# Optimization experiments

Hardware: AMD Instinct MI355X
Metric: run time of the kernel (lower is better)

The kernel has to match this reference:

```python
import jax, jax.numpy as jnp
import numpy as np

K = 128          # fixed max number of points per persistence diagram
BIG = 1e9        # sentinel for masked sort


def _extrema_masks(img):
    # 4-neighborhood local minima / maxima of a 2D image (boundary neighbors = +/-inf)
    p = jnp.pad(img, 1, constant_values=BIG)
    nmin = jnp.minimum(jnp.minimum(p[:-2, 1:-1], p[2:, 1:-1]),
                       jnp.minimum(p[1:-1, :-2], p[1:-1, 2:]))
    q = jnp.pad(img, 1, constant_values=-BIG)
    nmax = jnp.maximum(jnp.maximum(q[:-2, 1:-1], q[2:, 1:-1]),
                       jnp.maximum(q[1:-1, :-2], q[1:-1, 2:]))
    return img <= nmin, img >= nmax


def _diagrams(img):
    # Approximate persistence diagrams of the sublevel-set filtration of img.
    # H0: births at local minima (K smallest), deaths at local maxima (K smallest).
    # H1 (via superlevel duality approx): births at local maxima (K largest),
    #     deaths at local minima (K largest). Fixed cardinality K, invalid slots -> (0,0).
    is_min, is_max = _extrema_masks(img)
    flat = img.ravel()
    mn, mx = is_min.ravel(), is_max.ravel()

    b0 = jnp.sort(jnp.where(mn, flat, BIG))[:K]
    d0 = jnp.sort(jnp.where(mx, flat, BIG))[:K]
    v0 = (b0 < BIG / 2) & (d0 < BIG / 2)
    pd0 = jnp.where(v0[:, None], jnp.stack([b0, jnp.maximum(d0, b0)], -1), 0.0)

    b1 = -jnp.sort(jnp.where(mx, -flat, BIG))[:K]
    d1 = -jnp.sort(jnp.where(mn, -flat, BIG))[:K]
    v1 = (b1 > -BIG / 2) & (d1 > -BIG / 2)
    pd1 = jnp.where(v1[:, None], jnp.stack([b1, jnp.minimum(d1, b1)], -1), 0.0)
    return pd0, pd1


def _w2sq(pa, pb):
    # squared 2-Wasserstein with internal L2, matching points in sorted order
    # (sliced/order-matching approximation of the optimal diagram matching)
    return jnp.sum((pa - pb) ** 2)


def setup_inputs() -> dict:
    key = jax.random.key(0)
    k1, k2 = jax.random.split(key)
    inputs = jax.random.normal(k1, (256, 256, 256), dtype=jnp.float32)
    targets = jax.random.normal(k2, (256, 256, 256), dtype=jnp.float32)
    return {"inputs": inputs, "targets": targets}


def reference(inputs, targets):
    def per_sample(x, y):
        x0, x1 = _diagrams(x)
        y0, y1 = _diagrams(y)
        # wasserstein(pd0)^2 + wasserstein(pd1)^2, as in wasserstein_topological
        return _w2sq(x0, y0) + _w2sq(x1, y1)

    losses = jax.vmap(per_sample)(inputs, targets)  # [B]
    return jnp.mean(losses)  # reduction='mean'
```

## Files before the change

kernel.cpp:

```cpp
#include <hip/hip_runtime.h>
#include <stdint.h>


#define KPTS 128
#define BIGF 1.0e9f
#define IMG_W 256
#define NPIX (IMG_W * IMG_W)
#define NTH 1024
#define QITERS (NPIX / 4 / NTH)
#define LCAP 16384

__device__ __forceinline__ uint32_t f2key(float f) {
    uint32_t u = __float_as_uint(f);
    return (u & 0x80000000u) ? ~u : (u | 0x80000000u);
}
__device__ __forceinline__ float key2f(uint32_t k) {
    uint32_t u = (k & 0x80000000u) ? (k ^ 0x80000000u) : ~k;
    return __uint_as_float(u);
}


struct SMP {
    uint32_t keys[LCAP];
    uint32_t h8[8][256];
    uint32_t cnt[2];
    uint32_t pref[2], rank[2], ccnt[2];
    int      flagAll[2];
    float    buf[4][KPTS];
};

__device__ __forceinline__ void binSelN(const uint32_t (*h)[256], int ncop, int lane, uint32_t r,
                                        uint32_t& bsel, uint32_t& newr) {
    uint32_t b0 = 0, b1 = 0, b2 = 0, b3 = 0;
    for (int c = 0; c < ncop; ++c) {
        b0 += h[c][4 * lane];     b1 += h[c][4 * lane + 1];
        b2 += h[c][4 * lane + 2]; b3 += h[c][4 * lane + 3];
    }
    uint32_t s4 = b0 + b1 + b2 + b3, cum = s4;
    #pragma unroll
    for (int d = 1; d < 64; d <<= 1) { uint32_t t = __shfl_up(cum, d); if (lane >= d) cum += t; }
    unsigned long long m = __ballot(cum > r);
    int L = (m == 0ull) ? 63 : __builtin_ctzll(m);
    uint32_t cumL = __shfl(cum, L), s4L = __shfl(s4, L);
    uint32_t a0 = __shfl(b0, L), a1 = __shfl(b1, L), a2 = __shfl(b2, L);
    uint32_t excl = cumL - s4L;
    if (excl + a0 > r)                { bsel = 4u * L;     newr = r - excl; }
    else if (excl + a0 + a1 > r)      { bsel = 4u * L + 1; newr = r - excl - a0; }
    else if (excl + a0 + a1 + a2 > r) { bsel = 4u * L + 2; newr = r - excl - a0 - a1; }
    else                              { bsel = 4u * L + 3; newr = r - excl - a0 - a1 - a2; }
}

__device__ __forceinline__ void waveSort128(float e[2], bool asc, int lane) {
    for (int size = 2; size <= 128; size <<= 1) {
        for (int stride = size >> 1; stride > 0; stride >>= 1) {
            if (stride == 64) {
                float a = e[0], b = e[1];
                e[0] = asc ? fminf(a, b) : fmaxf(a, b);
                e[1] = asc ? fmaxf(a, b) : fminf(a, b);
            } else {
                #pragma unroll
                for (int r = 0; r < 2; ++r) {
                    int i = r * 64 + lane;
                    float v = e[r];
                    float w = __shfl_xor(v, stride);
                    bool up = ((i & size) == 0) ? asc : !asc;
                    bool lower = (i & stride) == 0;
                    float mn = fminf(v, w), mx = fmaxf(v, w);
                    e[r] = (lower == up) ? mn : mx;
                }
            }
        }
    }
}

__global__ __launch_bounds__(NTH, 8) void topo_pd4_kernel(
        const float* __restrict__ X, const float* __restrict__ Y,
        float* __restrict__ diagOut, uint32_t* __restrict__ gscr, int B) {
    __shared__ SMP sm;
    const int tid = threadIdx.x;
    const int lane = tid & 63;
    const int wv = tid >> 6;
    const int bid = blockIdx.x;
    const float* img = ((bid & 1) ? Y : X) + (size_t)(bid >> 1) * NPIX;
    uint32_t* gmax = gscr + (size_t)bid * LCAP;
    const unsigned long long ltm = (1ull << lane) - 1ull;

    for (int ph = 0; ph < 2; ++ph) {
        for (int i = tid; i < 8 * 256; i += NTH) ((uint32_t*)sm.h8)[i] = 0u;
        if (ph == 0 && tid < 2) sm.cnt[tid] = 0u;
        __syncthreads();
        uint32_t C;

        if (ph == 0) {
            for (int it = 0; it < QITERS; ++it) {
                int q = it * NTH + tid;
                int p = q * 4;
                int row = p >> 8;
                float4 cur = *(const float4*)(img + p);
                bool hu = row > 0, hd = row < (IMG_W - 1);
                float4 up = cur, dn = cur;
                if (hu) up = *(const float4*)(img + p - IMG_W);
                if (hd) dn = *(const float4*)(img + p + IMG_W);
                float lft = __shfl_up(cur.w, 1);
                float rgt = __shfl_down(cur.x, 1);
                bool hl = (lane > 0), hr = (lane < 63);
                float cv[4] = {cur.x, cur.y, cur.z, cur.w};
                float uv[4] = {up.x, up.y, up.z, up.w};
                float dv[4] = {dn.x, dn.y, dn.z, dn.w};
                bool mnf[4], mxf[4];
                uint32_t kk[4];
                #pragma unroll
                for (int j = 0; j < 4; ++j) {
                    float v = cv[j];
                    bool el = (j > 0) || hl, er = (j < 3) || hr;
                    float vl = (j > 0) ? cv[j - 1] : lft;
                    float vr = (j < 3) ? cv[j + 1] : rgt;
                    float nmn = fminf(fminf(el ? vl : BIGF, er ? vr : BIGF),
                                      fminf(hu ? uv[j] : BIGF, hd ? dv[j] : BIGF));
                    float nmx = fmaxf(fmaxf(el ? vl : -BIGF, er ? vr : -BIGF),
                                      fmaxf(hu ? uv[j] : -BIGF, hd ? dv[j] : -BIGF));
                    mnf[j] = (v <= nmn);
                    mxf[j] = (v >= nmx);
                    kk[j] = f2key(v);
                }
                {
                    unsigned long long m0 = __ballot(mnf[0]), m1 = __ballot(mnf[1]),
                                       m2 = __ballot(mnf[2]), m3 = __ballot(mnf[3]);
                    uint32_t c0 = (uint32_t)__popcll(m0), c1 = (uint32_t)__popcll(m1),
                             c2 = (uint32_t)__popcll(m2), c3 = (uint32_t)__popcll(m3);
                    uint32_t base = 0;
                    if (lane == 0) base = atomicAdd(&sm.cnt[0], c0 + c1 + c2 + c3);
                    base = __shfl(base, 0);
                    uint32_t o;
                    if (mnf[0]) { o = base + (uint32_t)__popcll(m0 & ltm);                sm.keys[o < LCAP ? o : LCAP - 1] = kk[0]; atomicAdd(&sm.h8[wv >> 1][kk[0] >> 24], 1u); }
                    if (mnf[1]) { o = base + c0 + (uint32_t)__popcll(m1 & ltm);           sm.keys[o < LCAP ? o : LCAP - 1] = kk[1]; atomicAdd(&sm.h8[wv >> 1][kk[1] >> 24], 1u); }
                    if (mnf[2]) { o = base + c0 + c1 + (uint32_t)__popcll(m2 & ltm);      sm.keys[o < LCAP ? o : LCAP - 1] = kk[2]; atomicAdd(&sm.h8[wv >> 1][kk[2] >> 24], 1u); }
                    if (mnf[3]) { o = base + c0 + c1 + c2 + (uint32_t)__popcll(m3 & ltm); sm.keys[o < LCAP ? o : LCAP - 1] = kk[3]; atomicAdd(&sm.h8[wv >> 1][kk[3] >> 24], 1u); }
                }
                {
                    unsigned long long m0 = __ballot(mxf[0]), m1 = __ballot(mxf[1]),
                                       m2 = __ballot(mxf[2]), m3 = __ballot(mxf[3]);
                    uint32_t c0 = (uint32_t)__popcll(m0), c1 = (uint32_t)__popcll(m1),
                             c2 = (uint32_t)__popcll(m2), c3 = (uint32_t)__popcll(m3);
                    uint32_t base = 0;
                    if (lane == 0) base = atomicAdd(&sm.cnt[1], c0 + c1 + c2 + c3);
                    base = __shfl(base, 0);
                    uint32_t o;
                    if (mxf[0]) { o = base + (uint32_t)__popcll(m0 & ltm);                gmax[o < LCAP ? o : LCAP - 1] = kk[0]; }
                    if (mxf[1]) { o = base + c0 + (uint32_t)__popcll(m1 & ltm);           gmax[o < LCAP ? o : LCAP - 1] = kk[1]; }
                    if (mxf[2]) { o = base + c0 + c1 + (uint32_t)__popcll(m2 & ltm);      gmax[o < LCAP ? o : LCAP - 1] = kk[2]; }
                    if (mxf[3]) { o = base + c0 + c1 + c2 + (uint32_t)__popcll(m3 & ltm); gmax[o < LCAP ? o : LCAP - 1] = kk[3]; }
                }
            }
            __syncthreads();
            C = sm.cnt[0]; if (C > LCAP) C = LCAP;
        } else {
            C = sm.cnt[1]; if (C > LCAP) C = LCAP;
            for (uint32_t i = tid; i < C; i += NTH) {
                uint32_t k = gmax[i];
                sm.keys[i] = k;
                atomicAdd(&sm.h8[wv >> 1][k >> 24], 1u);
            }
            __syncthreads();
        }

        if (wv < 2) {
            bool low = (wv == 0);
            if (C < KPTS) {
                if (lane == 0) { sm.flagAll[wv] = 1; sm.pref[wv] = 0u; sm.rank[wv] = 0u; }
            } else {
                uint32_t bsel, nr;
                binSelN(sm.h8, 8, lane, low ? (KPTS - 1) : (C - KPTS), bsel, nr);
                if (lane == 0) { sm.flagAll[wv] = 0; sm.pref[wv] = bsel; sm.rank[wv] = nr; }
            }
        }
        __syncthreads();

        for (int lvl = 2; lvl >= 0; --lvl) {
            for (int i = tid; i < 2 * 256; i += NTH) ((uint32_t*)sm.h8)[i] = 0u;
            __syncthreads();
            int f0 = sm.flagAll[0], f1 = sm.flagAll[1];
            uint32_t p0 = sm.pref[0], p1 = sm.pref[1];
            const int sp = 8 * (lvl + 1), sb = 8 * lvl;
            for (uint32_t i = tid; i < C; i += NTH) {
                uint32_t k = sm.keys[i], hi = k >> sp, by = (k >> sb) & 255u;
                if (!f0 && hi == p0) atomicAdd(&sm.h8[0][by], 1u);
                if (!f1 && hi == p1) atomicAdd(&sm.h8[1][by], 1u);
            }
            __syncthreads();
            if (wv < 2 && !sm.flagAll[wv]) {
                uint32_t bsel, nr;
                binSelN((const uint32_t(*)[256])&sm.h8[wv], 1, lane, sm.rank[wv], bsel, nr);
                if (lane == 0) { sm.pref[wv] = (sm.pref[wv] << 8) | bsel; sm.rank[wv] = nr; }
            }
            __syncthreads();
        }

        if (tid < 2) sm.ccnt[tid] = 0u;
        __syncthreads();
        const int g0 = (ph == 0) ? 0 : 1;
        const int g1 = (ph == 0) ? 3 : 2;
        {
            int f0 = sm.flagAll[0], f1 = sm.flagAll[1];
            uint32_t t0 = sm.pref[0], t1 = sm.pref[1];
            for (uint32_t i = tid; i < C; i += NTH) {
                uint32_t k = sm.keys[i];
                if (f0 || k < t0) { uint32_t s = atomicAdd(&sm.ccnt[0], 1u); if (s < KPTS) sm.buf[g0][s] = key2f(k); }
                if (f1 || k > t1) { uint32_t s = atomicAdd(&sm.ccnt[1], 1u); if (s < KPTS) sm.buf[g1][s] = key2f(k); }
            }
        }
        __syncthreads();
        if (tid < 2 * KPTS) {
            int l = tid >> 7, i = tid & 127;
            int g = (l == 0) ? g0 : g1;
            if ((uint32_t)i >= sm.ccnt[l])
                sm.buf[g][i] = sm.flagAll[l] ? ((l == 0) ? BIGF : -BIGF) : key2f(sm.pref[l]);
        }
        __syncthreads();
    }

    if (wv < 4) {
        float e[2];
        e[0] = sm.buf[wv][lane];
        e[1] = sm.buf[wv][lane + 64];
        waveSort128(e, wv < 2, lane);
        diagOut[(size_t)bid * 512 + wv * 128 + lane]      = e[0];
        diagOut[(size_t)bid * 512 + wv * 128 + 64 + lane] = e[1];
    }
}

__global__ __launch_bounds__(128) void topo_loss_kernel(
        const float* __restrict__ diag, float* __restrict__ lossOut, int B) {
    const int s = blockIdx.x, i = threadIdx.x;
    const float* xw = diag + (size_t)(2 * s) * 512;
    const float* yw = xw + 512;
    const float H = 0.5f * BIGF;
    float b0x = xw[i], d0x = xw[128 + i], b1x = xw[256 + i], d1x = xw[384 + i];
    float b0y = yw[i], d0y = yw[128 + i], b1y = yw[256 + i], d1y = yw[384 + i];
    bool vx0 = (b0x < H) && (d0x < H);
    float px0b = vx0 ? b0x : 0.f, px0d = vx0 ? fmaxf(d0x, b0x) : 0.f;
    bool vy0 = (b0y < H) && (d0y < H);
    float py0b = vy0 ? b0y : 0.f, py0d = vy0 ? fmaxf(d0y, b0y) : 0.f;
    bool vx1 = (b1x > -H) && (d1x > -H);
    float px1b = vx1 ? b1x : 0.f, px1d = vx1 ? fminf(d1x, b1x) : 0.f;
    bool vy1 = (b1y > -H) && (d1y > -H);
    float py1b = vy1 ? b1y : 0.f, py1d = vy1 ? fminf(d1y, b1y) : 0.f;
    float e0 = px0b - py0b, e1 = px0d - py0d, e2 = px1b - py1b, e3 = px1d - py1d;
    float total = e0 * e0 + e1 * e1 + e2 * e2 + e3 * e3;
    for (int off = 32; off; off >>= 1) total += __shfl_down(total, off);
    __shared__ float lr[2];
    if ((i & 63) == 0) lr[i >> 6] = total;
    __syncthreads();
    if (i == 0) lossOut[s] = lr[0] + lr[1];
}

__global__ void topo_reduce_kernel(const float* __restrict__ ws, float* __restrict__ out, int B) {
    float v = 0.f;
    for (int i = threadIdx.x; i < B; i += 256) v += ws[i];
    __shared__ float r[4];
    for (int off = 32; off; off >>= 1) v += __shfl_down(v, off);
    if ((threadIdx.x & 63) == 0) r[threadIdx.x >> 6] = v;
    __syncthreads();
    if (threadIdx.x == 0) out[0] = (r[0] + r[1] + r[2] + r[3]) / (float)B;
}

__global__ __launch_bounds__(NTH, 8) void topo_pd3_kernel(
        const float* __restrict__ X, const float* __restrict__ Y,
        float* __restrict__ diagOut, int B) {
    __shared__ SMP sm;
    const int tid = threadIdx.x;
    const int lane = tid & 63;
    const int wv = tid >> 6;
    const int bid = blockIdx.x;
    const float* img = ((bid & 1) ? Y : X) + (size_t)(bid >> 1) * NPIX;
    const unsigned long long ltm = (1ull << lane) - 1ull;

    for (int ph = 0; ph < 2; ++ph) {
        for (int i = tid; i < 8 * 256; i += NTH) ((uint32_t*)sm.h8)[i] = 0u;
        if (tid == 0) sm.cnt[0] = 0u;
        __syncthreads();
        for (int it = 0; it < QITERS; ++it) {
            int q = it * NTH + tid;
            int p = q * 4;
            int row = p >> 8;
            float4 cur = *(const float4*)(img + p);
            bool hu = row > 0, hd = row < (IMG_W - 1);
            float4 up = cur, dn = cur;
            if (hu) up = *(const float4*)(img + p - IMG_W);
            if (hd) dn = *(const float4*)(img + p + IMG_W);
            float lft = __shfl_up(cur.w, 1);
            float rgt = __shfl_down(cur.x, 1);
            bool hl = (lane > 0), hr = (lane < 63);
            float cv[4] = {cur.x, cur.y, cur.z, cur.w};
            float uv[4] = {up.x, up.y, up.z, up.w};
            float dv[4] = {dn.x, dn.y, dn.z, dn.w};
            bool e0, e1, e2, e3;
            if (ph == 0) {
                #define SMIN(J, E, EL, ER, VL, VR)                                        \
                    { float nm = fminf(fminf((EL) ? (VL) : BIGF, (ER) ? (VR) : BIGF),     \
                                       fminf(hu ? uv[J] : BIGF, hd ? dv[J] : BIGF));      \
                      E = (cv[J] <= nm); }
                SMIN(0, e0, hl, true, lft,  cv[1]);
                SMIN(1, e1, true, true, cv[0], cv[2]);
                SMIN(2, e2, true, true, cv[1], cv[3]);
                SMIN(3, e3, true, hr, cv[2], rgt);
                #undef SMIN
            } else {
                #define SMAX(J, E, EL, ER, VL, VR)                                        \
                    { float nx = fmaxf(fmaxf((EL) ? (VL) : -BIGF, (ER) ? (VR) : -BIGF),   \
                                       fmaxf(hu ? uv[J] : -BIGF, hd ? dv[J] : -BIGF));    \
                      E = (cv[J] >= nx); }
                SMAX(0, e0, hl, true, lft,  cv[1]);
                SMAX(1, e1, true, true, cv[0], cv[2]);
                SMAX(2, e2, true, true, cv[1], cv[3]);
                SMAX(3, e3, true, hr, cv[2], rgt);
                #undef SMAX
            }
            uint32_t k0 = f2key(cv[0]), k1 = f2key(cv[1]), k2 = f2key(cv[2]), k3 = f2key(cv[3]);
            unsigned long long m0 = __ballot(e0), m1 = __ballot(e1),
                               m2 = __ballot(e2), m3 = __ballot(e3);
            uint32_t c0 = (uint32_t)__popcll(m0), c1 = (uint32_t)__popcll(m1),
                     c2 = (uint32_t)__popcll(m2), c3 = (uint32_t)__popcll(m3);
            uint32_t base = 0;
            if (lane == 0) base = atomicAdd(&sm.cnt[0], c0 + c1 + c2 + c3);
            base = __shfl(base, 0);
            uint32_t o;
            if (e0) { o = base + (uint32_t)__popcll(m0 & ltm);                sm.keys[o < LCAP ? o : LCAP - 1] = k0; atomicAdd(&sm.h8[wv >> 1][k0 >> 24], 1u); }
            if (e1) { o = base + c0 + (uint32_t)__popcll(m1 & ltm);           sm.keys[o < LCAP ? o : LCAP - 1] = k1; atomicAdd(&sm.h8[wv >> 1][k1 >> 24], 1u); }
            if (e2) { o = base + c0 + c1 + (uint32_t)__popcll(m2 & ltm);      sm.keys[o < LCAP ? o : LCAP - 1] = k2; atomicAdd(&sm.h8[wv >> 1][k2 >> 24], 1u); }
            if (e3) { o = base + c0 + c1 + c2 + (uint32_t)__popcll(m3 & ltm); sm.keys[o < LCAP ? o : LCAP - 1] = k3; atomicAdd(&sm.h8[wv >> 1][k3 >> 24], 1u); }
        }
        __syncthreads();
        uint32_t C = sm.cnt[0]; if (C > LCAP) C = LCAP;

        if (wv < 2) {
            bool low = (wv == 0);
            if (C < KPTS) {
                if (lane == 0) { sm.flagAll[wv] = 1; sm.pref[wv] = 0u; sm.rank[wv] = 0u; }
            } else {
                uint32_t bsel, nr;
                binSelN(sm.h8, 8, lane, low ? (KPTS - 1) : (C - KPTS), bsel, nr);
                if (lane == 0) { sm.flagAll[wv] = 0; sm.pref[wv] = bsel; sm.rank[wv] = nr; }
            }
        }
        __syncthreads();

        for (int lvl = 2; lvl >= 0; --lvl) {
            for (int i = tid; i < 2 * 256; i += NTH) ((uint32_t*)sm.h8)[i] = 0u;
            __syncthreads();
            int f0 = sm.flagAll[0], f1 = sm.flagAll[1];
            uint32_t p0 = sm.pref[0], p1 = sm.pref[1];
            const int sp = 8 * (lvl + 1), sb = 8 * lvl;
            for (uint32_t i = tid; i < C; i += NTH) {
                uint32_t k = sm.keys[i], hi = k >> sp, by = (k >> sb) & 255u;
                if (!f0 && hi == p0) atomicAdd(&sm.h8[0][by], 1u);
                if (!f1 && hi == p1) atomicAdd(&sm.h8[1][by], 1u);
            }
            __syncthreads();
            if (wv < 2 && !sm.flagAll[wv]) {
                uint32_t bsel, nr;
                binSelN((const uint32_t(*)[256])&sm.h8[wv], 1, lane, sm.rank[wv], bsel, nr);
                if (lane == 0) { sm.pref[wv] = (sm.pref[wv] << 8) | bsel; sm.rank[wv] = nr; }
            }
            __syncthreads();
        }

        if (tid < 2) sm.ccnt[tid] = 0u;
        __syncthreads();
        const int g0 = (ph == 0) ? 0 : 1;
        const int g1 = (ph == 0) ? 3 : 2;
        {
            int f0 = sm.flagAll[0], f1 = sm.flagAll[1];
            uint32_t t0 = sm.pref[0], t1 = sm.pref[1];
            for (uint32_t i = tid; i < C; i += NTH) {
                uint32_t k = sm.keys[i];
                if (f0 || k < t0) { uint32_t s = atomicAdd(&sm.ccnt[0], 1u); if (s < KPTS) sm.buf[g0][s] = key2f(k); }
                if (f1 || k > t1) { uint32_t s = atomicAdd(&sm.ccnt[1], 1u); if (s < KPTS) sm.buf[g1][s] = key2f(k); }
            }
        }
        __syncthreads();
        if (tid < 2 * KPTS) {
            int l = tid >> 7, i = tid & 127;
            int g = (l == 0) ? g0 : g1;
            if ((uint32_t)i >= sm.ccnt[l])
                sm.buf[g][i] = sm.flagAll[l] ? ((l == 0) ? BIGF : -BIGF) : key2f(sm.pref[l]);
        }
        __syncthreads();
    }

    if (wv < 4) {
        float e[2];
        e[0] = sm.buf[wv][lane];
        e[1] = sm.buf[wv][lane + 64];
        waveSort128(e, wv < 2, lane);
        diagOut[(size_t)bid * 512 + wv * 128 + lane]      = e[0];
        diagOut[(size_t)bid * 512 + wv * 128 + 64 + lane] = e[1];
    }
}

extern "C" void kernel_launch(void* const* d_in, const int* in_sizes, int n_in,
                              void* d_out, int out_size, void* d_ws, size_t ws_size,
                              hipStream_t stream) {
    const float* X = (const float*)d_in[0];
    const float* Y = (const float*)d_in[1];
    float* out = (float*)d_out;
    const int B = in_sizes[0] / NPIX;

    size_t diagSz = (size_t)2 * B * 512 * sizeof(float);
    size_t lossSz = (size_t)B * sizeof(float);
    size_t scrSz  = (size_t)2 * B * LCAP * sizeof(uint32_t);

    if (ws_size >= diagSz + lossSz + scrSz) {
        float* diag = (float*)d_ws;
        float* lossbuf = (float*)((char*)d_ws + diagSz);
        uint32_t* gscr = (uint32_t*)((char*)d_ws + diagSz + lossSz);
        topo_pd4_kernel<<<2 * B, NTH, 0, stream>>>(X, Y, diag, gscr, B);
        topo_loss_kernel<<<B, 128, 0, stream>>>(diag, lossbuf, B);
        topo_reduce_kernel<<<1, 256, 0, stream>>>(lossbuf, out, B);
    } else if (ws_size >= diagSz + lossSz) {
        float* diag = (float*)d_ws;
        float* lossbuf = (float*)((char*)d_ws + diagSz);
        topo_pd3_kernel<<<2 * B, NTH, 0, stream>>>(X, Y, diag, B);
        topo_loss_kernel<<<B, 128, 0, stream>>>(diag, lossbuf, B);
        topo_reduce_kernel<<<1, 256, 0, stream>>>(lossbuf, out, B);
    } else {
        topo_pd3_kernel<<<2 * B, NTH, 0, stream>>>(X, Y, (float*)d_ws, B);
    }
}
```

Baseline: 91.87 us.

## Split extrema scan into grid-wide row kernel and separate selection kernel

The fused per-image kernel, where one 1024-thread block scanned a whole image and then ran radix select, is split in two. A row-parallel scan kernel with 2048 blocks of 256 threads writes the compacted min and max key lists to global memory using global atomic counters. A second kernel per image loads these lists, builds padded, lane-spread shared histograms and performs the selection. This aims to spread the bandwidth-bound scan across the whole GPU and cut shared-atomic contention, at the cost of an extra memset, an extra launch and a global round-trip for the min keys.

Result: slower. 350.6 us (+281.6%).

```diff
diff --git a/kernel.cpp b/kernel.cpp
--- a/kernel.cpp
+++ b/kernel.cpp
@@ -9,6 +9,7 @@
 #define NTH 1024
 #define QITERS (NPIX / 4 / NTH)
 #define LCAP 16384
+#define HPAD 264
 
 __device__ __forceinline__ uint32_t f2key(float f) {
     uint32_t u = __float_as_uint(f);
@@ -20,21 +21,83 @@
 }
 
 
-struct SMP {
+__global__ __launch_bounds__(256) void topo_scan_kernel(
+        const float* __restrict__ X, const float* __restrict__ Y,
+        uint32_t* __restrict__ gkeys, uint32_t* __restrict__ gcnt, int B) {
+    const int tid = threadIdx.x;
+    const int lane = tid & 63;
+    const int wv = tid >> 6;
+    const int gw = blockIdx.x * 4 + wv;
+    const int nw = gridDim.x * 4;
+    const int totalRows = 2 * B * IMG_W;
+    const unsigned long long ltm = (1ull << lane) - 1ull;
+
+    for (int r = gw; r < totalRows; r += nw) {
+        int im = r >> 8, row = r & 255;
+        const float* base = ((im & 1) ? Y : X) + (size_t)(im >> 1) * NPIX + (size_t)row * IMG_W;
+        float4 cur = *(const float4*)(base + lane * 4);
+        bool hu = row > 0, hd = row < (IMG_W - 1);
+        float4 up = cur, dn = cur;
+        if (hu) up = *(const float4*)(base - IMG_W + lane * 4);
+        if (hd) dn = *(const float4*)(base + IMG_W + lane * 4);
+        float lft = __shfl_up(cur.w, 1);
+        float rgt = __shfl_down(cur.x, 1);
+        bool hl = (lane > 0), hr = (lane < 63);
+        float cv[4] = {cur.x, cur.y, cur.z, cur.w};
+        float uv[4] = {up.x, up.y, up.z, up.w};
+        float dv[4] = {dn.x, dn.y, dn.z, dn.w};
+        bool mnf[4], mxf[4];
+        uint32_t kk[4];
+        #pragma unroll
+        for (int j = 0; j < 4; ++j) {
+            float v = cv[j];
+            bool el = (j > 0) || hl, er = (j < 3) || hr;
+            float vl = (j > 0) ? cv[j - 1] : lft;
+            float vr = (j < 3) ? cv[j + 1] : rgt;
+            float nmn = fminf(fminf(el ? vl : BIGF, er ? vr : BIGF),
+                              fminf(hu ? uv[j] : BIGF, hd ? dv[j] : BIGF));
+            float nmx = fmaxf(fmaxf(el ? vl : -BIGF, er ? vr : -BIGF),
+                              fmaxf(hu ? uv[j] : -BIGF, hd ? dv[j] : -BIGF));
+            mnf[j] = (v <= nmn);
+            mxf[j] = (v >= nmx);
+            kk[j] = f2key(v);
+        }
+        #pragma unroll
+        for (int t = 0; t < 2; ++t) {
+            bool f0 = t ? mxf[0] : mnf[0], f1 = t ? mxf[1] : mnf[1];
+            bool f2 = t ? mxf[2] : mnf[2], f3 = t ? mxf[3] : mnf[3];
+            unsigned long long m0 = __ballot(f0), m1 = __ballot(f1),
+                               m2 = __ballot(f2), m3 = __ballot(f3);
+            uint32_t c0 = (uint32_t)__popcll(m0), c1 = (uint32_t)__popcll(m1),
+                     c2 = (uint32_t)__popcll(m2), c3 = (uint32_t)__popcll(m3);
+            uint32_t bse = 0;
+            if (lane == 0) bse = atomicAdd(&gcnt[im * 2 + t], c0 + c1 + c2 + c3);
+            bse = __shfl(bse, 0);
+            uint32_t* dst = gkeys + (size_t)(im * 2 + t) * LCAP;
+            uint32_t o;
+            if (f0) { o = bse + (uint32_t)__popcll(m0 & ltm);                dst[o < LCAP ? o : LCAP - 1] = kk[0]; }
+            if (f1) { o = bse + c0 + (uint32_t)__popcll(m1 & ltm);           dst[o < LCAP ? o : LCAP - 1] = kk[1]; }
+            if (f2) { o = bse + c0 + c1 + (uint32_t)__popcll(m2 & ltm);      dst[o < LCAP ? o : LCAP - 1] = kk[2]; }
+            if (f3) { o = bse + c0 + c1 + c2 + (uint32_t)__popcll(m3 & ltm); dst[o < LCAP ? o : LCAP - 1] = kk[3]; }
+        }
+    }
+}
+
+struct SMQ {
     uint32_t keys[LCAP];
-    uint32_t h8[8][256];
-    uint32_t cnt[2];
+    uint32_t h8[8 * HPAD];
     uint32_t pref[2], rank[2], ccnt[2];
     int      flagAll[2];
     float    buf[4][KPTS];
 };
 
-__device__ __forceinline__ void binSelN(const uint32_t (*h)[256], int ncop, int lane, uint32_t r,
+__device__ __forceinline__ void binSelP(const uint32_t* h, int ncop, int lane, uint32_t r,
                                         uint32_t& bsel, uint32_t& newr) {
     uint32_t b0 = 0, b1 = 0, b2 = 0, b3 = 0;
     for (int c = 0; c < ncop; ++c) {
-        b0 += h[c][4 * lane];     b1 += h[c][4 * lane + 1];
-        b2 += h[c][4 * lane + 2]; b3 += h[c][4 * lane + 3];
+        const uint32_t* hh = h + c * HPAD;
+        b0 += hh[4 * lane];     b1 += hh[4 * lane + 1];
+        b2 += hh[4 * lane + 2]; b3 += hh[4 * lane + 3];
     }
     uint32_t s4 = b0 + b1 + b2 + b3, cum = s4;
     #pragma unroll
@@ -73,96 +136,28 @@
     }
 }
 
-__global__ __launch_bounds__(NTH, 8) void topo_pd4_kernel(
-        const float* __restrict__ X, const float* __restrict__ Y,
-        float* __restrict__ diagOut, uint32_t* __restrict__ gscr, int B) {
-    __shared__ SMP sm;
+__global__ __launch_bounds__(NTH, 8) void topo_sel_kernel(
+        const uint32_t* __restrict__ gkeys, const uint32_t* __restrict__ gcnt,
+        float* __restrict__ diagOut, int B) {
+    __shared__ SMQ sm;
     const int tid = threadIdx.x;
     const int lane = tid & 63;
     const int wv = tid >> 6;
-    const int bid = blockIdx.x;
-    const float* img = ((bid & 1) ? Y : X) + (size_t)(bid >> 1) * NPIX;
-    uint32_t* gmax = gscr + (size_t)bid * LCAP;
-    const unsigned long long ltm = (1ull << lane) - 1ull;
+    const int im = blockIdx.x;
+    const int hc = lane & 7;
 
     for (int ph = 0; ph < 2; ++ph) {
-        for (int i = tid; i < 8 * 256; i += NTH) ((uint32_t*)sm.h8)[i] = 0u;
-        if (ph == 0 && tid < 2) sm.cnt[tid] = 0u;
-        __syncthreads();
-        uint32_t C;
-
-        if (ph == 0) {
-            for (int it = 0; it < QITERS; ++it) {
-                int q = it * NTH + tid;
-                int p = q * 4;
-                int row = p >> 8;
-                float4 cur = *(const float4*)(img + p);
-                bool hu = row > 0, hd = row < (IMG_W - 1);
-                float4 up = cur, dn = cur;
-                if (hu) up = *(const float4*)(img + p - IMG_W);
-                if (hd) dn = *(const float4*)(img + p + IMG_W);
-                float lft = __shfl_up(cur.w, 1);
-                float rgt = __shfl_down(cur.x, 1);
-                bool hl = (lane > 0), hr = (lane < 63);
-                float cv[4] = {cur.x, cur.y, cur.z, cur.w};
-                float uv[4] = {up.x, up.y, up.z, up.w};
-                float dv[4] = {dn.x, dn.y, dn.z, dn.w};
-                bool mnf[4], mxf[4];
-                uint32_t kk[4];
-                #pragma unroll
-                for (int j = 0; j < 4; ++j) {
-                    float v = cv[j];
-                    bool el = (j > 0) || hl, er = (j < 3) || hr;
-                    float vl = (j > 0) ? cv[j - 1] : lft;
-                    float vr = (j < 3) ? cv[j + 1] : rgt;
-                    float nmn = fminf(fminf(el ? vl : BIGF, er ? vr : BIGF),
-                                      fminf(hu ? uv[j] : BIGF, hd ? dv[j] : BIGF));
-                    float nmx = fmaxf(fmaxf(el ? vl : -BIGF, er ? vr : -BIGF),
-                                      fmaxf(hu ? uv[j] : -BIGF, hd ? dv[j] : -BIGF));
-                    mnf[j] = (v <= nmn);
-                    mxf[j] = (v >= nmx);
-                    kk[j] = f2key(v);
-                }
-                {
-                    unsigned long long m0 = __ballot(mnf[0]), m1 = __ballot(mnf[1]),
-                                       m2 = __ballot(mnf[2]), m3 = __ballot(mnf[3]);
-                    uint32_t c0 = (uint32_t)__popcll(m0), c1 = (uint32_t)__popcll(m1),
-                             c2 = (uint32_t)__popcll(m2), c3 = (uint32_t)__popcll(m3);
-                    uint32_t base = 0;
-                    if (lane == 0) base = atomicAdd(&sm.cnt[0], c0 + c1 + c2 + c3);
-                    base = __shfl(base, 0);
-                    uint32_t o;
-                    if (mnf[0]) { o = base + (uint32_t)__popcll(m0 & ltm);                sm.keys[o < LCAP ? o : LCAP - 1] = kk[0]; atomicAdd(&sm.h8[wv >> 1][kk[0] >> 24], 1u); }
-                    if (mnf[1]) { o = base + c0 + (uint32_t)__popcll(m1 & ltm);           sm.keys[o < LCAP ? o : LCAP - 1] = kk[1]; atomicAdd(&sm.h8[wv >> 1][kk[1] >> 24], 1u); }
-                    if (mnf[2]) { o = base + c0 + c1 + (uint32_t)__popcll(m2 & ltm);      sm.keys[o < LCAP ? o : LCAP - 1] = kk[2]; atomicAdd(&sm.h8[wv >> 1][kk[2] >> 24], 1u); }
-                    if (mnf[3]) { o = base + c0 + c1 + c2 + (uint32_t)__popcll(m3 & ltm); sm.keys[o < LCAP ? o : LCAP - 1] = kk[3]; atomicAdd(&sm.h8[wv >> 1][kk[3] >> 24], 1u); }
-                }
-                {
-                    unsigned long long m0 = __ballot(mxf[0]), m1 = __ballot(mxf[1]),
-                                       m2 = __ballot(mxf[2]), m3 = __ballot(mxf[3]);
-                    uint32_t c0 = (uint32_t)__popcll(m0), c1 = (uint32_t)__popcll(m1),
-                             c2 = (uint32_t)__popcll(m2), c3 = (uint32_t)__popcll(m3);
-                    uint32_t base = 0;
-                    if (lane == 0) base = atomicAdd(&sm.cnt[1], c0 + c1 + c2 + c3);
-                    base = __shfl(base, 0);
-                    uint32_t o;
-                    if (mxf[0]) { o = base + (uint32_t)__popcll(m0 & ltm);                gmax[o < LCAP ? o : LCAP - 1] = kk[0]; }
-                    if (mxf[1]) { o = base + c0 + (uint32_t)__popcll(m1 & ltm);           gmax[o < LCAP ? o : LCAP - 1] = kk[1]; }
-                    if (mxf[2]) { o = base + c0 + c1 + (uint32_t)__popcll(m2 & ltm);      gmax[o < LCAP ? o : LCAP - 1] = kk[2]; }
-                    if (mxf[3]) { o = base + c0 + c1 + c2 + (uint32_t)__popcll(m3 & ltm); gmax[o < LCAP ? o : LCAP - 1] = kk[3]; }
-                }
-            }
-            __syncthreads();
-            C = sm.cnt[0]; if (C > LCAP) C = LCAP;
-        } else {
-            C = sm.cnt[1]; if (C > LCAP) C = LCAP;
-            for (uint32_t i = tid; i < C; i += NTH) {
-                uint32_t k = gmax[i];
-                sm.keys[i] = k;
-                atomicAdd(&sm.h8[wv >> 1][k >> 24], 1u);
-            }
-            __syncthreads();
-        }
+        for (int i = tid; i < 8 * HPAD; i += NTH) sm.h8[i] = 0u;
+        __syncthreads();
+        const uint32_t* list = gkeys + (size_t)(im * 2 + ph) * LCAP;
+        uint32_t C = gcnt[im * 2 + ph]; if (C > LCAP) C = LCAP;
+
+        for (uint32_t i = tid; i < C; i += NTH) {
+            uint32_t k = list[i];
+            sm.keys[i] = k;
+            atomicAdd(&sm.h8[hc * HPAD + (k >> 24)], 1u);
+        }
+        __syncthreads();
 
         if (wv < 2) {
             bool low = (wv == 0);
@@ -170,27 +165,27 @@
                 if (lane == 0) { sm.flagAll[wv] = 1; sm.pref[wv] = 0u; sm.rank[wv] = 0u; }
             } else {
                 uint32_t bsel, nr;
-                binSelN(sm.h8, 8, lane, low ? (KPTS - 1) : (C - KPTS), bsel, nr);
+                binSelP(sm.h8, 8, lane, low ? (KPTS - 1) : (C - KPTS), bsel, nr);
                 if (lane == 0) { sm.flagAll[wv] = 0; sm.pref[wv] = bsel; sm.rank[wv] = nr; }
             }
         }
         __syncthreads();
 
         for (int lvl = 2; lvl >= 0; --lvl) {
-            for (int i = tid; i < 2 * 256; i += NTH) ((uint32_t*)sm.h8)[i] = 0u;
+            for (int i = tid; i < 2 * HPAD; i += NTH) sm.h8[i] = 0u;
             __syncthreads();
             int f0 = sm.flagAll[0], f1 = sm.flagAll[1];
             uint32_t p0 = sm.pref[0], p1 = sm.pref[1];
             const int sp = 8 * (lvl + 1), sb = 8 * lvl;
             for (uint32_t i = tid; i < C; i += NTH) {
                 uint32_t k = sm.keys[i], hi = k >> sp, by = (k >> sb) & 255u;
-                if (!f0 && hi == p0) atomicAdd(&sm.h8[0][by], 1u);
-                if (!f1 && hi == p1) atomicAdd(&sm.h8[1][by], 1u);
+                if (!f0 && hi == p0) atomicAdd(&sm.h8[by], 1u);
+                if (!f1 && hi == p1) atomicAdd(&sm.h8[HPAD + by], 1u);
             }
             __syncthreads();
             if (wv < 2 && !sm.flagAll[wv]) {
                 uint32_t bsel, nr;
-                binSelN((const uint32_t(*)[256])&sm.h8[wv], 1, lane, sm.rank[wv], bsel, nr);
+                binSelP(&sm.h8[wv * HPAD], 1, lane, sm.rank[wv], bsel, nr);
                 if (lane == 0) { sm.pref[wv] = (sm.pref[wv] << 8) | bsel; sm.rank[wv] = nr; }
             }
             __syncthreads();
@@ -224,8 +219,8 @@
         e[0] = sm.buf[wv][lane];
         e[1] = sm.buf[wv][lane + 64];
         waveSort128(e, wv < 2, lane);
-        diagOut[(size_t)bid * 512 + wv * 128 + lane]      = e[0];
-        diagOut[(size_t)bid * 512 + wv * 128 + 64 + lane] = e[1];
+        diagOut[(size_t)im * 512 + wv * 128 + lane]      = e[0];
+        diagOut[(size_t)im * 512 + wv * 128 + 64 + lane] = e[1];
     }
 }
 
@@ -262,6 +257,36 @@
     if ((threadIdx.x & 63) == 0) r[threadIdx.x >> 6] = v;
     __syncthreads();
     if (threadIdx.x == 0) out[0] = (r[0] + r[1] + r[2] + r[3]) / (float)B;
+}
+
+struct SMP {
+    uint32_t keys[LCAP];
+    uint32_t h8[8][256];
+    uint32_t cnt[2];
+    uint32_t pref[2], rank[2], ccnt[2];
+    int      flagAll[2];
+    float    buf[4][KPTS];
+};
+
+__device__ __forceinline__ void binSelN(const uint32_t (*h)[256], int ncop, int lane, uint32_t r,
+                                        uint32_t& bsel, uint32_t& newr) {
+    uint32_t b0 = 0, b1 = 0, b2 = 0, b3 = 0;
+    for (int c = 0; c < ncop; ++c) {
+        b0 += h[c][4 * lane];     b1 += h[c][4 * lane + 1];
+        b2 += h[c][4 * lane + 2]; b3 += h[c][4 * lane + 3];
+    }
+    uint32_t s4 = b0 + b1 + b2 + b3, cum = s4;
+    #pragma unroll
+    for (int d = 1; d < 64; d <<= 1) { uint32_t t = __shfl_up(cum, d); if (lane >= d) cum += t; }
+    unsigned long long m = __ballot(cum > r);
+    int L = (m == 0ull) ? 63 : __builtin_ctzll(m);
+    uint32_t cumL = __shfl(cum, L), s4L = __shfl(s4, L);
+    uint32_t a0 = __shfl(b0, L), a1 = __shfl(b1, L), a2 = __shfl(b2, L);
+    uint32_t excl = cumL - s4L;
+    if (excl + a0 > r)                { bsel = 4u * L;     newr = r - excl; }
+    else if (excl + a0 + a1 > r)      { bsel = 4u * L + 1; newr = r - excl - a0; }
+    else if (excl + a0 + a1 + a2 > r) { bsel = 4u * L + 2; newr = r - excl - a0 - a1; }
+    else                              { bsel = 4u * L + 3; newr = r - excl - a0 - a1 - a2; }
 }
 
 __global__ __launch_bounds__(NTH, 8) void topo_pd3_kernel(
@@ -408,13 +433,17 @@
 
     size_t diagSz = (size_t)2 * B * 512 * sizeof(float);
     size_t lossSz = (size_t)B * sizeof(float);
-    size_t scrSz  = (size_t)2 * B * LCAP * sizeof(uint32_t);
-
-    if (ws_size >= diagSz + lossSz + scrSz) {
+    size_t cntSz  = (size_t)2 * B * 2 * sizeof(uint32_t);
+    size_t keysSz = (size_t)2 * B * 2 * LCAP * sizeof(uint32_t);
+
+    if (ws_size >= diagSz + lossSz + cntSz + keysSz) {
         float* diag = (float*)d_ws;
         float* lossbuf = (float*)((char*)d_ws + diagSz);
-        uint32_t* gscr = (uint32_t*)((char*)d_ws + diagSz + lossSz);
-        topo_pd4_kernel<<<2 * B, NTH, 0, stream>>>(X, Y, diag, gscr, B);
+        uint32_t* gcnt = (uint32_t*)((char*)d_ws + diagSz + lossSz);
+        uint32_t* gkeys = (uint32_t*)((char*)d_ws + diagSz + lossSz + cntSz);
+        hipMemsetAsync(gcnt, 0, cntSz, stream);
+        topo_scan_kernel<<<2048, 256, 0, stream>>>(X, Y, gkeys, gcnt, B);
+        topo_sel_kernel<<<2 * B, NTH, 0, stream>>>(gkeys, gcnt, diag, B);
         topo_loss_kernel<<<B, 128, 0, stream>>>(diag, lossbuf, B);
         topo_reduce_kernel<<<1, 256, 0, stream>>>(lossbuf, out, B);
     } else if (ws_size >= diagSz + lossSz) {
```
